# Optimization experiments

Hardware: AMD Instinct MI355X
Metric: run time of the kernel (lower is better)

## Reference

```python
import jax, jax.numpy as jnp
import numpy as np

N = 10000; E = 160000; NF = 5; EF = 3; H = 8; C = 128; HC = H * C; G = 16

def _glorot(key, shape):
    s = float(np.sqrt(6.0 / (shape[0] + shape[-1])))
    return jax.random.uniform(key, shape, minval=-s, maxval=s, dtype=jnp.float32)

def setup_inputs():
    key = jax.random.key(0)
    ks = jax.random.split(key, 32)
    inp = {}
    inp["x"] = jax.random.normal(ks[0], (N, NF), dtype=jnp.float32)
    inp["edge_index"] = jax.random.randint(ks[1], (2, E), 0, N, dtype=jnp.int32)
    inp["edge_attr"] = jax.random.normal(ks[2], (E, EF), dtype=jnp.float32)
    inp["batch"] = jnp.sort(jax.random.randint(ks[3], (N,), 0, G, dtype=jnp.int32))
    ins = [NF, HC, HC, HC]
    i = 4
    for l in range(4):
        inp[f"W{l+1}"] = _glorot(ks[i], (ins[l], HC)); i += 1
        inp[f"We{l+1}"] = _glorot(ks[i], (EF, HC)); i += 1
        inp[f"as{l+1}"] = _glorot(ks[i], (H, C)); i += 1
        inp[f"ad{l+1}"] = _glorot(ks[i], (H, C)); i += 1
        inp[f"ae{l+1}"] = _glorot(ks[i], (H, C)); i += 1
        inp[f"b{l+1}"] = jnp.zeros((HC if l < 3 else C,), jnp.float32)
    inp["lin_w"] = _glorot(ks[i], (C, 1)) * 2.0
    inp["lin_b"] = jnp.zeros((1,), jnp.float32)
    return inp

def _gat(x, src, dst, ea, W, We, a_s, a_d, a_e, bias, concat):
    # PyG GATConv with edge_dim, add_self_loops=True, fill_value='mean'
    n = x.shape[0]
    cnt = jax.ops.segment_sum(jnp.ones((src.shape[0],), x.dtype), dst, n)
    loop_attr = jax.ops.segment_sum(ea, dst, n) / jnp.maximum(cnt, 1.0)[:, None]
    sl = jnp.arange(n, dtype=src.dtype)
    src2 = jnp.concatenate([src, sl])
    dst2 = jnp.concatenate([dst, sl])
    ea2 = jnp.concatenate([ea, loop_attr], axis=0)
    xl = (x @ W).reshape(n, H, C)                       # [N,H,C]
    a_src = jnp.einsum("nhc,hc->nh", xl, a_s)
    a_dst = jnp.einsum("nhc,hc->nh", xl, a_d)
    el = (ea2 @ We).reshape(-1, H, C)                    # [E2,H,C]
    alpha = a_src[src2] + a_dst[dst2] + jnp.einsum("ehc,hc->eh", el, a_e)
    alpha = jax.nn.leaky_relu(alpha, 0.2)
    m = jax.ops.segment_max(alpha, dst2, n)
    m = jnp.where(jnp.isfinite(m), m, 0.0)
    ex = jnp.exp(alpha - m[dst2])
    den = jax.ops.segment_sum(ex, dst2, n)
    alpha = ex / (den[dst2] + 1e-16)                     # segment softmax over dst
    out = jax.ops.segment_sum(alpha[:, :, None] * xl[src2], dst2, n)  # [N,H,C]
    if concat:
        return out.reshape(n, HC) + bias
    return out.mean(axis=1) + bias

def reference(x, edge_index, edge_attr, batch,
              W1, We1, as1, ad1, ae1, b1,
              W2, We2, as2, ad2, ae2, b2,
              W3, We3, as3, ad3, ae3, b3,
              W4, We4, as4, ad4, ae4, b4,
              lin_w, lin_b):
    src, dst = edge_index[0], edge_index[1]
    h = jax.nn.elu(_gat(x, src, dst, edge_attr, W1, We1, as1, ad1, ae1, b1, True))
    h = jax.nn.elu(_gat(h, src, dst, edge_attr, W2, We2, as2, ad2, ae2, b2, True))
    h = jax.nn.elu(_gat(h, src, dst, edge_attr, W3, We3, as3, ad3, ae3, b3, True))
    h = jax.nn.elu(_gat(h, src, dst, edge_attr, W4, We4, as4, ad4, ae4, b4, False))
    cnt = jax.ops.segment_sum(jnp.ones((N,), h.dtype), batch, G)
    pooled = jax.ops.segment_sum(h, batch, G) / jnp.maximum(cnt, 1.0)[:, None]
    return (pooled @ lin_w + lin_b).squeeze(-1)
```

## Files before the change

kernel.cpp:

```cpp
#include <hip/hip_runtime.h>
#include <math.h>

#define Nn 10000
#define En 160000
#define NF 5
#define EF 3
#define Hh 8
#define Cc 128
#define HC 1024
#define Gg 16

#define Mpad 10112

typedef __attribute__((ext_vector_type(8))) _Float16 half8;
typedef __attribute__((ext_vector_type(4))) float f32x4;


__device__ __forceinline__ void gl_lds16(const void* g, void* l) {
    __builtin_amdgcn_global_load_lds((const __attribute__((address_space(1))) void*)g,
                                     (__attribute__((address_space(3))) void*)l, 16, 0, 0);
}

__device__ __forceinline__ float elu_f(float v) {
    return (v > 0.f) ? v : expm1f(v);
}


__global__ void deg_sum_k(const int* __restrict__ dst, const float* __restrict__ ea,
                          int* __restrict__ cnt, float* __restrict__ sum_ea) {
    int e = blockIdx.x * 256 + threadIdx.x;
    if (e >= En) return;
    int d = dst[e];
    atomicAdd(&cnt[d], 1);
    atomicAdd(&sum_ea[d * 3 + 0], ea[e * 3 + 0]);
    atomicAdd(&sum_ea[d * 3 + 1], ea[e * 3 + 1]);
    atomicAdd(&sum_ea[d * 3 + 2], ea[e * 3 + 2]);
}

__global__ __launch_bounds__(1024) void scan_k(const int* __restrict__ cnt,
                                               int* __restrict__ rowptr,
                                               int* __restrict__ fillptr,
                                               float* __restrict__ loop_attr,
                                               const int* __restrict__ batch,
                                               int* __restrict__ gstart) {
    __shared__ int sh[1024];
    int tid = threadIdx.x;
    int base = tid * 10;
    int loc[10];
    int tsum = 0;
#pragma unroll
    for (int j = 0; j < 10; ++j) {
        int i = base + j;
        int v = 0;
        if (i < Nn) {
            v = cnt[i];
            float s = 1.0f / fmaxf((float)v, 1.0f);
            loop_attr[i * 3 + 0] *= s;
            loop_attr[i * 3 + 1] *= s;
            loop_attr[i * 3 + 2] *= s;
        }
        loc[j] = tsum;
        tsum += v;
    }
    sh[tid] = tsum;
    __syncthreads();
    for (int off = 1; off < 1024; off <<= 1) {
        int t = (tid >= off) ? sh[tid - off] : 0;
        __syncthreads();
        sh[tid] += t;
        __syncthreads();
    }
    int excl = sh[tid] - tsum;
#pragma unroll
    for (int j = 0; j < 10; ++j) {
        int i = base + j;
        if (i < Nn) {
            rowptr[i] = excl + loc[j];
            fillptr[i] = excl + loc[j];
        }
    }
    if (tid == 1023) rowptr[Nn] = sh[1023];
#pragma unroll
    for (int j = 0; j < 10; ++j) {
        int i = base + j;
        if (i < Nn) {
            int b = batch[i];
            if (i == 0) {
                for (int g = 0; g <= b; ++g) gstart[g] = 0;
            } else {
                int pb = batch[i - 1];
                for (int g = pb + 1; g <= b; ++g) gstart[g] = i;
            }
            if (i == Nn - 1) {
                for (int g = b + 1; g <= Gg; ++g) gstart[g] = Nn;
            }
        }
    }
}

__global__ void csr_fill_k(const int* __restrict__ src, const int* __restrict__ dst,
                           const float* __restrict__ ea, int* __restrict__ fillptr,
                           float4* __restrict__ eaP) {
    int e = blockIdx.x * 256 + threadIdx.x;
    if (e >= En) return;
    int d = dst[e];
    int pos = atomicAdd(&fillptr[d], 1);
    eaP[pos] = make_float4(ea[e * 3 + 0], ea[e * 3 + 1], ea[e * 3 + 2],
                           __int_as_float(src[e]));
}


__global__ void wae_all_k(const float* __restrict__ We1, const float* __restrict__ ae1,
                          const float* __restrict__ We2, const float* __restrict__ ae2,
                          const float* __restrict__ We3, const float* __restrict__ ae3,
                          const float* __restrict__ We4, const float* __restrict__ ae4,
                          float* __restrict__ w_ae_all) {
    int t = threadIdx.x;
    if (t >= 96) return;
    int l = t / 24, idx = t % 24;
    int f = idx >> 3, h = idx & 7;
    const float* We = (l == 0) ? We1 : (l == 1) ? We2 : (l == 2) ? We3 : We4;
    const float* ae = (l == 0) ? ae1 : (l == 1) ? ae2 : (l == 2) ? ae3 : ae4;
    float s = 0.f;
    for (int c = 0; c < Cc; ++c) s += We[f * HC + h * Cc + c] * ae[h * Cc + c];
    w_ae_all[l * 24 + f * 8 + h] = s;
}

__global__ __launch_bounds__(1024) void wsplit_all_k(const float* __restrict__ W2,
                                                     const float* __restrict__ W3,
                                                     const float* __restrict__ W4,
                                                     _Float16* __restrict__ Wt16) {
    __shared__ float tile[32][33];
    int z = blockIdx.z;
    const float* W = (z == 0) ? W2 : (z == 1) ? W3 : W4;
    int nb = blockIdx.x * 32, kb = blockIdx.y * 32;
    tile[threadIdx.y][threadIdx.x] = W[(size_t)(kb + threadIdx.y) * HC + nb + threadIdx.x];
    __syncthreads();
    float x = tile[threadIdx.x][threadIdx.y];
    int n = nb + threadIdx.y, k = kb + threadIdx.x;
    Wt16[(size_t)z * HC * HC + (size_t)n * HC + k] = (_Float16)x;
}


__global__ void gemm_k5(const float* __restrict__ x, const float* __restrict__ Wm,
                        const float* __restrict__ a_s, const float* __restrict__ a_d,
                        _Float16* __restrict__ out16,
                        float* __restrict__ a_srcB, float* __restrict__ a_dstB) {
    int n = blockIdx.x;
    int tid = threadIdx.x;
    __shared__ float xr[8];
    __shared__ float vrow[HC];
    if (tid < NF) xr[tid] = x[n * NF + tid];
    __syncthreads();
    float x0 = xr[0], x1 = xr[1], x2 = xr[2], x3 = xr[3], x4 = xr[4];
    for (int j = tid; j < HC; j += 256) {
        float v = x0 * Wm[j] + x1 * Wm[HC + j] + x2 * Wm[2 * HC + j]
                + x3 * Wm[3 * HC + j] + x4 * Wm[4 * HC + j];
        out16[(size_t)n * HC + j] = (_Float16)v;
        vrow[j] = v;
    }
    __syncthreads();
    int w = tid >> 6, lane = tid & 63;
#pragma unroll
    for (int q = 0; q < 2; ++q) {
        int h = w * 2 + q;
        float v0 = vrow[h * Cc + lane], v1 = vrow[h * Cc + 64 + lane];
        float s1 = v0 * a_s[h * Cc + lane] + v1 * a_s[h * Cc + 64 + lane];
        float s2 = v0 * a_d[h * Cc + lane] + v1 * a_d[h * Cc + 64 + lane];
#pragma unroll
        for (int off = 32; off; off >>= 1) {
            s1 += __shfl_xor(s1, off);
            s2 += __shfl_xor(s2, off);
        }
        if (lane == 0) { a_srcB[n * 8 + h] = s1; a_dstB[n * 8 + h] = s2; }
    }
}

__global__ __launch_bounds__(256) void gemm_mfma(const _Float16* __restrict__ A,
                                                 const _Float16* __restrict__ Bt,
                                                 const float* __restrict__ a_s,
                                                 const float* __restrict__ a_d,
                                                 _Float16* __restrict__ C16,
                                                 float* __restrict__ a_srcB,
                                                 float* __restrict__ a_dstB) {
    __shared__ _Float16 As[128 * 32];
    __shared__ _Float16 Bs[128 * 32];
    __shared__ float ps[128][2];
    __shared__ float pd[128][2];
    int tid = threadIdx.x;
    int wave = tid >> 6, lane = tid & 63;
    int wr = wave >> 1, wc = wave & 1;
    int row0 = blockIdx.y * 128;
    int col0 = blockIdx.x * 128;
    int h = blockIdx.x;

    f32x4 acc[4][4];
#pragma unroll
    for (int i = 0; i < 4; ++i)
#pragma unroll
        for (int j = 0; j < 4; ++j) acc[i][j] = (f32x4){0.f, 0.f, 0.f, 0.f};

    int srow = lane >> 2;
    int scol = (lane & 3) * 8;
    int fr = lane & 15;
    int fk = (lane >> 4) * 8;

    for (int kb = 0; kb < 1024; kb += 32) {
#pragma unroll
        for (int cc = 0; cc < 2; ++cc) {
            int c = wave + cc * 4;
            int r = c * 16 + srow;
            gl_lds16(A + (size_t)(row0 + r) * 1024 + kb + scol, &As[c * 512 + lane * 8]);
            gl_lds16(Bt + (size_t)(col0 + r) * 1024 + kb + scol, &Bs[c * 512 + lane * 8]);
        }
        __syncthreads();

        half8 af[4], bf[4];
#pragma unroll
        for (int i = 0; i < 4; ++i)
            af[i] = *(const half8*)&As[(wr * 64 + i * 16 + fr) * 32 + fk];
#pragma unroll
        for (int j = 0; j < 4; ++j)
            bf[j] = *(const half8*)&Bs[(wc * 64 + j * 16 + fr) * 32 + fk];
#pragma unroll
        for (int i = 0; i < 4; ++i)
#pragma unroll
            for (int j = 0; j < 4; ++j)
                acc[i][j] = __builtin_amdgcn_mfma_f32_16x16x32_f16(af[i], bf[j], acc[i][j],
                                                                   0, 0, 0);
        __syncthreads();
    }

    int cn = lane & 15, rq = (lane >> 4) * 4;
#pragma unroll
    for (int i = 0; i < 4; ++i) {
        int rbase = row0 + wr * 64 + i * 16 + rq;
#pragma unroll
        for (int j = 0; j < 4; ++j) {
            int col = col0 + wc * 64 + j * 16 + cn;
#pragma unroll
            for (int r = 0; r < 4; ++r) {
                int row = rbase + r;
                if (row < Nn) C16[(size_t)row * HC + col] = (_Float16)acc[i][j][r];
            }
        }
    }
    float asv[4], adv[4];
#pragma unroll
    for (int j = 0; j < 4; ++j) {
        int c = wc * 64 + j * 16 + cn;
        asv[j] = a_s[h * Cc + c];
        adv[j] = a_d[h * Cc + c];
    }
#pragma unroll
    for (int i = 0; i < 4; ++i)
#pragma unroll
        for (int r = 0; r < 4; ++r) {
            float rs = acc[i][0][r] * asv[0] + acc[i][1][r] * asv[1]
                     + acc[i][2][r] * asv[2] + acc[i][3][r] * asv[3];
            float rd = acc[i][0][r] * adv[0] + acc[i][1][r] * adv[1]
                     + acc[i][2][r] * adv[2] + acc[i][3][r] * adv[3];
#pragma unroll
            for (int off = 1; off < 16; off <<= 1) {
                rs += __shfl_xor(rs, off);
                rd += __shfl_xor(rd, off);
            }
            if (cn == 0) {
                int rib = wr * 64 + i * 16 + rq + r;
                ps[rib][wc] = rs;
                pd[rib][wc] = rd;
            }
        }
    __syncthreads();
    if (tid < 128) {
        int row = row0 + tid;
        if (row < Nn) {
            a_srcB[row * 8 + h] = ps[tid][0] + ps[tid][1];
            a_dstB[row * 8 + h] = pd[tid][0] + pd[tid][1];
        }
    }
}


__global__ __launch_bounds__(256) void aggregate_k(const _Float16* __restrict__ xl16,
                                                   const float4* __restrict__ eaP,
                                                   const float* __restrict__ loop_attr,
                                                   const float* __restrict__ a_srcB,
                                                   const float* __restrict__ a_dstB,
                                                   const float* __restrict__ w_ae,
                                                   const int* __restrict__ rowptr,
                                                   const float* __restrict__ bias,
                                                   const float* __restrict__ lin_w,
                                                   _Float16* __restrict__ A2,
                                                   float* __restrict__ dnode,
                                                   int raw_mode) {
    int n = (blockIdx.x * 256 + threadIdx.x) >> 6;
    int lane = threadIdx.x & 63;
    if (n >= Nn) return;
    int beg = rowptr[n], end = rowptr[n + 1];
    int hc = lane >> 3;

    float w0c = w_ae[hc], w1c = w_ae[8 + hc], w2c = w_ae[16 + hc];
    float adst_n = a_dstB[n * 8 + hc];
    float asrc_n = a_srcB[n * 8 + hc];
    float f0 = loop_attr[n * 3 + 0], f1 = loop_attr[n * 3 + 1], f2 = loop_attr[n * 3 + 2];
    float av = asrc_n + adst_n + f0 * w0c + f1 * w1c + f2 * w2c;
    float aself = (av > 0.f) ? av : 0.2f * av;

    float acc[16];
    float s = 1.0f;
    {
        const _Float16* r = xl16 + (size_t)n * HC + lane * 16;
        half8 r0 = *(const half8*)r;
        half8 r1 = *(const half8*)(r + 8);
#pragma unroll
        for (int j = 0; j < 8; ++j) {
            acc[j] = (float)r0[j];
            acc[8 + j] = (float)r1[j];
        }
    }
    int loff = lane * 16;
    for (int i0 = beg; i0 < end; i0 += 4) {
        int last = end - 1;
        bool v1 = (i0 + 1 < end), v2 = (i0 + 2 < end), v3 = (i0 + 3 < end);
        int i1 = v1 ? i0 + 1 : last;
        int i2 = v2 ? i0 + 2 : last;
        int i3 = v3 ? i0 + 3 : last;
        float4 e0 = eaP[i0], e1 = eaP[i1], e2 = eaP[i2], e3 = eaP[i3];
        int s0 = __float_as_int(e0.w), s1 = __float_as_int(e1.w);
        int s2 = __float_as_int(e2.w), s3 = __float_as_int(e3.w);
        float as0 = a_srcB[s0 * 8 + hc], as1 = a_srcB[s1 * 8 + hc];
        float as2 = a_srcB[s2 * 8 + hc], as3 = a_srcB[s3 * 8 + hc];
        const _Float16* p0 = xl16 + (size_t)s0 * HC + loff;
        const _Float16* p1 = xl16 + (size_t)s1 * HC + loff;
        const _Float16* p2 = xl16 + (size_t)s2 * HC + loff;
        const _Float16* p3 = xl16 + (size_t)s3 * HC + loff;
        half8 q0a = *(const half8*)p0, q0b = *(const half8*)(p0 + 8);
        half8 q1a = *(const half8*)p1, q1b = *(const half8*)(p1 + 8);
        half8 q2a = *(const half8*)p2, q2b = *(const half8*)(p2 + 8);
        half8 q3a = *(const half8*)p3, q3b = *(const half8*)(p3 + 8);
        float al0 = as0 + adst_n + e0.x * w0c + e0.y * w1c + e0.z * w2c;
        float al1 = as1 + adst_n + e1.x * w0c + e1.y * w1c + e1.z * w2c;
        float al2 = as2 + adst_n + e2.x * w0c + e2.y * w1c + e2.z * w2c;
        float al3 = as3 + adst_n + e3.x * w0c + e3.y * w1c + e3.z * w2c;
        al0 = (al0 > 0.f) ? al0 : 0.2f * al0;
        al1 = (al1 > 0.f) ? al1 : 0.2f * al1;
        al2 = (al2 > 0.f) ? al2 : 0.2f * al2;
        al3 = (al3 > 0.f) ? al3 : 0.2f * al3;
        float u0 = __expf(al0 - aself);
        float u1 = v1 ? __expf(al1 - aself) : 0.f;
        float u2 = v2 ? __expf(al2 - aself) : 0.f;
        float u3 = v3 ? __expf(al3 - aself) : 0.f;
        s += u0 + u1 + u2 + u3;
#pragma unroll
        for (int j = 0; j < 8; ++j) {
            float t0 = acc[j], t1 = acc[8 + j];
            t0 = fmaf(u0, (float)q0a[j], t0);  t1 = fmaf(u0, (float)q0b[j], t1);
            t0 = fmaf(u1, (float)q1a[j], t0);  t1 = fmaf(u1, (float)q1b[j], t1);
            t0 = fmaf(u2, (float)q2a[j], t0);  t1 = fmaf(u2, (float)q2b[j], t1);
            t0 = fmaf(u3, (float)q3a[j], t0);  t1 = fmaf(u3, (float)q3b[j], t1);
            acc[j] = t0; acc[8 + j] = t1;
        }
    }
    float inv = 1.f / (s + 1e-16f);

    if (!raw_mode) {
        int ch = loff;
        half8 hv0, hv1;
#pragma unroll
        for (int j = 0; j < 8; ++j) {
            hv0[j] = (_Float16)elu_f(fmaf(acc[j], inv, bias[ch + j]));
            hv1[j] = (_Float16)elu_f(fmaf(acc[8 + j], inv, bias[ch + 8 + j]));
        }
        _Float16* p = A2 + (size_t)n * 1024 + ch;
        *(half8*)p = hv0;
        *(half8*)(p + 8) = hv1;
    } else {
#pragma unroll
        for (int j = 0; j < 16; ++j) acc[j] *= inv;
#pragma unroll
        for (int off = 8; off < 64; off <<= 1)
#pragma unroll
            for (int j = 0; j < 16; ++j) acc[j] += __shfl_xor(acc[j], off);
        int c0 = (lane & 7) * 16;
        float partial = 0.f;
#pragma unroll
        for (int j = 0; j < 16; ++j) {
            float v = elu_f(acc[j] * 0.125f + bias[c0 + j]);
            partial = fmaf(v, lin_w[c0 + j], partial);
        }
#pragma unroll
        for (int off = 1; off < 8; off <<= 1) partial += __shfl_xor(partial, off);
        if (lane == 0) dnode[n] = partial;
    }
}


__global__ __launch_bounds__(256) void pool_final_k(const float* __restrict__ dnode,
                                                    const int* __restrict__ gstart,
                                                    const float* __restrict__ lin_b,
                                                    float* __restrict__ out) {
    __shared__ float sh[256];
    int g = blockIdx.x;
    int tid = threadIdx.x;
    int s = gstart[g], e = gstart[g + 1];
    float acc = 0.f;
    for (int n = s + tid; n < e; n += 256) acc += dnode[n];
    sh[tid] = acc;
    __syncthreads();
    for (int off = 128; off; off >>= 1) {
        if (tid < off) sh[tid] += sh[tid + off];
        __syncthreads();
    }
    if (tid == 0) out[g] = sh[0] / fmaxf((float)(e - s), 1.f) + lin_b[0];
}


extern "C" void kernel_launch(void* const* d_in, const int* in_sizes, int n_in,
                              void* d_out, int out_size, void* d_ws, size_t ws_size,
                              hipStream_t stream) {
    const float* x = (const float*)d_in[0];
    const int* ei = (const int*)d_in[1];
    const float* ea = (const float*)d_in[2];
    const int* batch = (const int*)d_in[3];
    const float *Wl[4], *Wel[4], *asl[4], *adl[4], *ael[4], *bl[4];
    for (int l = 0; l < 4; ++l) {
        Wl[l] = (const float*)d_in[4 + 6 * l];
        Wel[l] = (const float*)d_in[5 + 6 * l];
        asl[l] = (const float*)d_in[6 + 6 * l];
        adl[l] = (const float*)d_in[7 + 6 * l];
        ael[l] = (const float*)d_in[8 + 6 * l];
        bl[l] = (const float*)d_in[9 + 6 * l];
    }
    const float* lin_w = (const float*)d_in[28];
    const float* lin_b = (const float*)d_in[29];
    const int* srcA = ei;
    const int* dstA = ei + En;

    float* Wp = (float*)d_ws;
    size_t o = 0;
    _Float16* A2 = (_Float16*)(Wp + o); o += (size_t)Mpad * 512;
    _Float16* Wt16 = (_Float16*)(Wp + o); o += (size_t)3 * HC * HC / 2;
    _Float16* xl16 = (_Float16*)(Wp + o); o += (size_t)Nn * HC / 2;
    float4* eaP = (float4*)(Wp + o); o += (size_t)En * 4;
    float* loop_attr = Wp + o; o += Nn * 3;
    int* cnt = (int*)(Wp + o); o += Nn;
    int* rowptr = (int*)(Wp + o); o += Nn + 1;
    int* fillptr = (int*)(Wp + o); o += Nn;
    int* gstart = (int*)(Wp + o); o += Gg + 1;
    float* a_srcB = Wp + o; o += Nn * Hh;
    float* a_dstB = Wp + o; o += Nn * Hh;
    float* w_ae_all = Wp + o; o += 128;
    float* dnode = Wp + o; o += Nn;

    hipMemsetAsync(cnt, 0, Nn * sizeof(int), stream);
    hipMemsetAsync(loop_attr, 0, Nn * 3 * sizeof(float), stream);

    deg_sum_k<<<(En + 255) / 256, 256, 0, stream>>>(dstA, ea, cnt, loop_attr);
    scan_k<<<1, 1024, 0, stream>>>(cnt, rowptr, fillptr, loop_attr, batch, gstart);
    csr_fill_k<<<(En + 255) / 256, 256, 0, stream>>>(srcA, dstA, ea, fillptr, eaP);
    wae_all_k<<<1, 128, 0, stream>>>(Wel[0], ael[0], Wel[1], ael[1], Wel[2], ael[2],
                                     Wel[3], ael[3], w_ae_all);
    wsplit_all_k<<<dim3(32, 32, 3), dim3(32, 32), 0, stream>>>(Wl[1], Wl[2], Wl[3], Wt16);

    for (int l = 0; l < 4; ++l) {
        if (l == 0)
            gemm_k5<<<Nn, 256, 0, stream>>>(x, Wl[0], asl[0], adl[0], xl16, a_srcB, a_dstB);
        else
            gemm_mfma<<<dim3(HC / 128, Mpad / 128), 256, 0, stream>>>(
                A2, Wt16 + (size_t)(l - 1) * HC * HC, asl[l], adl[l], xl16, a_srcB, a_dstB);
        aggregate_k<<<(Nn + 3) / 4, 256, 0, stream>>>(xl16, eaP, loop_attr, a_srcB,
                                                      a_dstB, w_ae_all + l * 24, rowptr,
                                                      bl[l], lin_w, A2, dnode,
                                                      (l == 3) ? 1 : 0);
    }
    pool_final_k<<<Gg, 256, 0, stream>>>(dnode, gstart, lin_b, (float*)d_out);
}
```

Before: 589.2 us.

## Split each node's edge aggregation across four wavefronts with LDS reduction

The aggregation kernel now assigns one 256-thread block per destination node instead of one wavefront per node. The four wavefronts each take an interleaved quarter of the node's incoming edges, and their partial accumulators and softmax denominators are combined through shared memory by wavefront 0. The aim is more memory-level parallelism and shorter per-node latency chains for the gather-heavy loop. In exchange it adds a block barrier and an LDS reduction, and grid occupancy is wasted when degrees are small (about 16 edges on average).

```diff
diff --git a/kernel.cpp b/kernel.cpp
--- a/kernel.cpp
+++ b/kernel.cpp
@@ -294,9 +294,11 @@
                                                    _Float16* __restrict__ A2,
                                                    float* __restrict__ dnode,
                                                    int raw_mode) {
-    int n = (blockIdx.x * 256 + threadIdx.x) >> 6;
+    __shared__ float cmbA[3][1024];
+    __shared__ float cmbS[3][64];
+    int sub = threadIdx.x >> 6;
     int lane = threadIdx.x & 63;
-    if (n >= Nn) return;
+    int n = blockIdx.x;
     int beg = rowptr[n], end = rowptr[n + 1];
     int hc = lane >> 3;
 
@@ -308,9 +310,10 @@
     float aself = (av > 0.f) ? av : 0.2f * av;
 
     float acc[16];
-    float s = 1.0f;
-    {
-        const _Float16* r = xl16 + (size_t)n * HC + lane * 16;
+    float s;
+    int loff = lane * 16;
+    if (sub == 0) {
+        const _Float16* r = xl16 + (size_t)n * HC + loff;
         half8 r0 = *(const half8*)r;
         half8 r1 = *(const half8*)(r + 8);
 #pragma unroll
@@ -318,14 +321,18 @@
             acc[j] = (float)r0[j];
             acc[8 + j] = (float)r1[j];
         }
-    }
-    int loff = lane * 16;
-    for (int i0 = beg; i0 < end; i0 += 4) {
-        int last = end - 1;
-        bool v1 = (i0 + 1 < end), v2 = (i0 + 2 < end), v3 = (i0 + 3 < end);
-        int i1 = v1 ? i0 + 1 : last;
-        int i2 = v2 ? i0 + 2 : last;
-        int i3 = v3 ? i0 + 3 : last;
+        s = 1.0f;
+    } else {
+#pragma unroll
+        for (int j = 0; j < 16; ++j) acc[j] = 0.f;
+        s = 0.0f;
+    }
+
+    for (int i0 = beg + sub; i0 < end; i0 += 16) {
+        bool v1 = (i0 + 4 < end), v2 = (i0 + 8 < end), v3 = (i0 + 12 < end);
+        int i1 = v1 ? i0 + 4 : i0;
+        int i2 = v2 ? i0 + 8 : i0;
+        int i3 = v3 ? i0 + 12 : i0;
         float4 e0 = eaP[i0], e1 = eaP[i1], e2 = eaP[i2], e3 = eaP[i3];
         int s0 = __float_as_int(e0.w), s1 = __float_as_int(e1.w);
         int s2 = __float_as_int(e2.w), s3 = __float_as_int(e3.w);
@@ -362,6 +369,28 @@
             acc[j] = t0; acc[8 + j] = t1;
         }
     }
+
+    if (sub != 0) {
+#pragma unroll
+        for (int j = 0; j < 4; ++j)
+            *(float4*)&cmbA[sub - 1][loff + j * 4] = *(const float4*)&acc[j * 4];
+        cmbS[sub - 1][lane] = s;
+    }
+    __syncthreads();
+    if (sub != 0) return;
+
+#pragma unroll
+    for (int k = 0; k < 3; ++k) {
+        s += cmbS[k][lane];
+#pragma unroll
+        for (int j = 0; j < 4; ++j) {
+            float4 c4 = *(const float4*)&cmbA[k][loff + j * 4];
+            acc[j * 4 + 0] += c4.x;
+            acc[j * 4 + 1] += c4.y;
+            acc[j * 4 + 2] += c4.z;
+            acc[j * 4 + 3] += c4.w;
+        }
+    }
     float inv = 1.f / (s + 1e-16f);
 
     if (!raw_mode) {
@@ -469,10 +498,10 @@
         else
             gemm_mfma<<<dim3(HC / 128, Mpad / 128), 256, 0, stream>>>(
                 A2, Wt16 + (size_t)(l - 1) * HC * HC, asl[l], adl[l], xl16, a_srcB, a_dstB);
-        aggregate_k<<<(Nn + 3) / 4, 256, 0, stream>>>(xl16, eaP, loop_attr, a_srcB,
-                                                      a_dstB, w_ae_all + l * 24, rowptr,
-                                                      bl[l], lin_w, A2, dnode,
-                                                      (l == 3) ? 1 : 0);
+        aggregate_k<<<Nn, 256, 0, stream>>>(xl16, eaP, loop_attr, a_srcB,
+                                            a_dstB, w_ae_all + l * 24, rowptr,
+                                            bl[l], lin_w, A2, dnode,
+                                            (l == 3) ? 1 : 0);
     }
     pool_final_k<<<Gg, 256, 0, stream>>>(dnode, gstart, lin_b, (float*)d_out);
 }
```

Result: faster. 564.9 us (median of 2 runs) (-4.1%).
